# Kernel tuning notes

Measured on AMD Instinct MI355X. Metric: run time of the kernel, lower is better.

The kernel has to match this reference:

```python
import jax, jax.numpy as jnp
import numpy as np

M, N, NNZ, NITER = 1_000_000, 1_000_000, 8_000_000, 5


def setup_inputs() -> dict:
    key = jax.random.key(0)
    ks = jax.random.split(key, 24)
    f32 = jnp.float32
    inp = dict(
        rows=jax.random.randint(ks[0], (NNZ,), 0, M, dtype=jnp.int32),
        cols=jax.random.randint(ks[1], (NNZ,), 0, N, dtype=jnp.int32),
        vals=jax.random.normal(ks[2], (NNZ,), dtype=f32) * 0.1,
        b=jax.random.normal(ks[3], (M, 1), dtype=f32),
        c=jax.random.normal(ks[4], (N, 1), dtype=f32),
        solution=jax.random.normal(ks[5], (N, 1), dtype=f32),
        dual_solution=jax.random.normal(ks[6], (M, 1), dtype=f32),
        x0=jax.random.normal(ks[7], (N, 1), dtype=f32),  # beta=1 init
        y0=jax.random.normal(ks[8], (M, 1), dtype=f32),  # std_y=1 init
        # dual tower: Conv1d(10->4), Conv1d(6->4), update Conv1d(6->1)
        dw1=jax.random.normal(ks[9], (4, 10), dtype=f32) * 0.3,
        db1=jax.random.normal(ks[10], (4,), dtype=f32) * 0.1,
        dw2=jax.random.normal(ks[11], (4, 6), dtype=f32) * 0.3,
        db2=jax.random.normal(ks[12], (4,), dtype=f32) * 0.1,
        dwu=jax.random.normal(ks[13], (1, 6), dtype=f32) * 0.1,
        dbu=jax.random.normal(ks[14], (1,), dtype=f32) * 0.1,
        # primal tower: Conv1d(10->4), Conv1d(6->4), update Conv1d(6->1)
        pw1=jax.random.normal(ks[15], (4, 10), dtype=f32) * 0.3,
        pb1=jax.random.normal(ks[16], (4,), dtype=f32) * 0.1,
        pw2=jax.random.normal(ks[17], (4, 6), dtype=f32) * 0.3,
        pb2=jax.random.normal(ks[18], (4,), dtype=f32) * 0.1,
        pwu=jax.random.normal(ks[19], (1, 6), dtype=f32) * 0.1,
        pbu=jax.random.normal(ks[20], (1,), dtype=f32) * 0.1,
        nb_max_iter=NITER,
    )
    return inp


def reference(rows, cols, vals, b, c, solution, dual_solution, x0, y0,
              dw1, db1, dw2, db2, dwu, dbu,
              pw1, pb1, pw2, pb2, pwu, pbu, nb_max_iter):
    m, n = b.shape[0], c.shape[0]

    def A_mm(X):   # sparse A @ X : [n,k] -> [m,k]
        return jax.ops.segment_sum(vals[:, None] * X[cols], rows, num_segments=m)

    def At_mm(Y):  # sparse A.T @ Y : [m,k] -> [n,k]
        return jax.ops.segment_sum(vals[:, None] * Y[rows], cols, num_segments=n)

    def step(carry, _):
        x, y, x_h, y_h = carry  # x[n,1] y[m,1] x_h[4,n] y_h[4,m]
        # dual update
        r = A_mm(x) - b                                   # [m,1]
        atxh = A_mm(x_h.T)                                # [m,4]
        h = jnp.concatenate([y_h, atxh.T, y.T, r.T], 0)   # [10,m]
        h = jax.nn.relu(dw1 @ h + db1[:, None])           # [4,m]
        h = jnp.concatenate([h, y.T, r.T], 0)             # [6,m]
        y_h = jax.nn.relu(dw2 @ h + db2[:, None])         # [4,m]
        h2 = jnp.concatenate([y_h, y.T, r.T], 0)          # [6,m]
        y = y + (dwu @ h2 + dbu[:, None]).T               # [m,1]
        # primal update
        d = c + At_mm(y)                                  # [n,1]
        atyh = At_mm(y_h.T)                               # [n,4]
        g = jnp.concatenate([x_h, atyh.T, x.T, d.T], 0)   # [10,n]
        g = jax.nn.relu(pw1 @ g + pb1[:, None])           # [4,n]
        g = jnp.concatenate([g, x.T, d.T], 0)             # [6,n]
        x_h = jax.nn.relu(pw2 @ g + pb2[:, None])         # [4,n]
        g2 = jnp.concatenate([x_h, x.T, d.T], 0)          # [6,n]
        x = x + (pwu @ g2 + pbu[:, None]).T               # [n,1]
        dp = jnp.sqrt(jnp.sum((x - solution) ** 2))
        dd = jnp.sqrt(jnp.sum((y - dual_solution) ** 2))
        return (x, y, x_h, y_h), (dp, dd)

    init = (x0, y0,
            jnp.zeros((4, n), dtype=x0.dtype),
            jnp.zeros((4, m), dtype=y0.dtype))
    (x, y, _, _), (dps, dds) = jax.lax.scan(step, init, None, length=nb_max_iter)

    loss_primal = jnp.mean(dps) + 1.0 * jnp.mean(jax.nn.relu(dps[1:] - dps[:-1]))
    loss_dual = jnp.mean(dds) + 1.0 * jnp.mean(jax.nn.relu(dds[1:] - dds[:-1]))
    loss = loss_primal + loss_dual
    return x, y, loss, dps, dds
```

## Files before the change

kernel.cpp:

```cpp
#include <hip/hip_runtime.h>
#include <math.h>


#define NITER 5
#define NBK_SHIFT 9
#define NBK (1 << NBK_SHIFT)
#define NBK_MAX 2048
#define CH 32768
#define SORT_CAP 6144

__device__ __forceinline__ float blockReduceSum(float v) {
#pragma unroll
  for (int off = 32; off > 0; off >>= 1) v += __shfl_down(v, off, 64);
  __shared__ float smem[8];
  const int lane = threadIdx.x & 63;
  const int wid = threadIdx.x >> 6;
  if (lane == 0) smem[wid] = v;
  __syncthreads();
  float r = 0.f;
  if (threadIdx.x == 0) {
    const int nw = (blockDim.x + 63) >> 6;
    for (int w = 0; w < nw; ++w) r += smem[w];
  }
  return r;
}

__global__ __launch_bounds__(1024) void zero_meta(int* __restrict__ cntA,
                                                  int* __restrict__ cntT,
                                                  float* __restrict__ red) {
  const int i = threadIdx.x;
  cntA[i] = 0;
  cntA[i + 1024] = 0;
  cntT[i] = 0;
  cntT[i + 1024] = 0;
  if (i < 16) red[i] = 0.f;
}

__global__ __launch_bounds__(256) void hist2(const int* __restrict__ rows,
                                             const int* __restrict__ cols,
                                             int* __restrict__ cntA,
                                             int* __restrict__ cntT, int nnz) {
  __shared__ int hA[NBK_MAX];
  __shared__ int hT[NBK_MAX];
  for (int i = threadIdx.x; i < NBK_MAX; i += 256) { hA[i] = 0; hT[i] = 0; }
  __syncthreads();
  const int stride = gridDim.x * blockDim.x;
  for (int e = blockIdx.x * blockDim.x + threadIdx.x; e < nnz; e += stride) {
    atomicAdd(&hA[rows[e] >> NBK_SHIFT], 1);
    atomicAdd(&hT[cols[e] >> NBK_SHIFT], 1);
  }
  __syncthreads();
  for (int i = threadIdx.x; i < NBK_MAX; i += 256) {
    if (hA[i]) atomicAdd(&cntA[i], hA[i]);
    if (hT[i]) atomicAdd(&cntT[i], hT[i]);
  }
}

__global__ __launch_bounds__(1024) void scan_bases(const int* __restrict__ cnt,
                                                   int* __restrict__ base,
                                                   int* __restrict__ fill,
                                                   int nb) {
  __shared__ int sm[1024];
  int run = 0;
  for (int s = 0; s < nb; s += 1024) {
    const int i = s + threadIdx.x;
    const int x = (i < nb) ? cnt[i] : 0;
    sm[threadIdx.x] = x;
    __syncthreads();
#pragma unroll
    for (int off = 1; off < 1024; off <<= 1) {
      const int add = (threadIdx.x >= off) ? sm[threadIdx.x - off] : 0;
      __syncthreads();
      sm[threadIdx.x] += add;
      __syncthreads();
    }
    if (i < nb) {
      const int ex = run + sm[threadIdx.x] - x;
      base[i] = ex;
      fill[i] = ex;
    }
    const int tot = sm[1023];
    __syncthreads();
    run += tot;
  }
}

__global__ __launch_bounds__(512) void scatter2(
    const int* __restrict__ rows, const int* __restrict__ cols,
    const float* __restrict__ vals, int* __restrict__ fillA,
    int* __restrict__ fillT, int2* __restrict__ eA, int2* __restrict__ eT,
    int nnz) {
  __shared__ int hA[NBK_MAX];
  __shared__ int hT[NBK_MAX];
  for (int i = threadIdx.x; i < NBK_MAX; i += 512) { hA[i] = 0; hT[i] = 0; }
  __syncthreads();
  const int e0 = blockIdx.x * CH;
  for (int k = threadIdx.x; k < CH; k += 512) {
    const int e = e0 + k;
    if (e < nnz) {
      atomicAdd(&hA[rows[e] >> NBK_SHIFT], 1);
      atomicAdd(&hT[cols[e] >> NBK_SHIFT], 1);
    }
  }
  __syncthreads();
  for (int i = threadIdx.x; i < NBK_MAX; i += 512) {
    const int cA = hA[i];
    if (cA) hA[i] = atomicAdd(&fillA[i], cA);
    const int cT = hT[i];
    if (cT) hT[i] = atomicAdd(&fillT[i], cT);
  }
  __syncthreads();
  for (int k = threadIdx.x; k < CH; k += 512) {
    const int e = e0 + k;
    if (e < nnz) {
      const int r = rows[e];
      const int c = cols[e];
      const int vb = __float_as_int(vals[e]);
      const int pA = atomicAdd(&hA[r >> NBK_SHIFT], 1);
      eA[pA] = make_int2(((r & (NBK - 1)) << 20) | c, vb);
      const int pT = atomicAdd(&hT[c >> NBK_SHIFT], 1);
      eT[pT] = make_int2(((c & (NBK - 1)) << 20) | r, vb);
    }
  }
}

__global__ __launch_bounds__(256) void sort_bucket(const int* __restrict__ base,
                                                   const int* __restrict__ cnt,
                                                   int2* __restrict__ edges) {
  __shared__ int2 recs[SORT_CAP];
  __shared__ int hist[NBK];
  __shared__ int wsum[256];
  const int bkt = blockIdx.x;
  const int beg = base[bkt];
  const int num = cnt[bkt];
  if (num > SORT_CAP) return;
  for (int i = threadIdx.x; i < NBK; i += 256) hist[i] = 0;
  __syncthreads();
  for (int k = threadIdx.x; k < num; k += 256) {
    const int2 r = edges[beg + k];
    recs[k] = r;
    atomicAdd(&hist[((unsigned)r.x) >> 20], 1);
  }
  __syncthreads();
  const int b2 = threadIdx.x * 2;
  const int h0 = hist[b2];
  const int h1 = hist[b2 + 1];
  wsum[threadIdx.x] = h0 + h1;
  __syncthreads();
#pragma unroll
  for (int off = 1; off < 256; off <<= 1) {
    const int add = (threadIdx.x >= off) ? wsum[threadIdx.x - off] : 0;
    __syncthreads();
    wsum[threadIdx.x] += add;
    __syncthreads();
  }
  const int excl = (threadIdx.x == 0) ? 0 : wsum[threadIdx.x - 1];
  __syncthreads();
  hist[b2] = excl;
  hist[b2 + 1] = excl + h0;
  __syncthreads();
  for (int k = threadIdx.x; k < num; k += 256) {
    const int2 r = recs[k];
    const int p = atomicAdd(&hist[((unsigned)r.x) >> 20], 1);
    edges[beg + p] = r;
  }
}

__global__ __launch_bounds__(256) void init_state2(const float* __restrict__ x0,
                                                   const float* __restrict__ y0,
                                                   float* __restrict__ X5,
                                                   float* __restrict__ Y5,
                                                   int n, int m) {
  const int i = blockIdx.x * blockDim.x + threadIdx.x;
  if (i < n) {
    float* xp = X5 + (size_t)i * 8;
    xp[0] = x0[i];
    xp[1] = 0.f; xp[2] = 0.f; xp[3] = 0.f; xp[4] = 0.f;
  }
  if (i < m) {
    float* yp = Y5 + (size_t)i * 8;
    yp[0] = y0[i];
    yp[1] = 0.f; yp[2] = 0.f; yp[3] = 0.f; yp[4] = 0.f;
  }
}

__global__ __launch_bounds__(256) void fused_bucket_tower(
    const int* __restrict__ base, const int* __restrict__ cnt,
    const int2* __restrict__ edges, const float* __restrict__ src,
    float* __restrict__ state, const float* __restrict__ seed, float sign,
    const float* __restrict__ sol, const float* __restrict__ w1,
    const float* __restrict__ b1, const float* __restrict__ w2,
    const float* __restrict__ b2, const float* __restrict__ wu,
    const float* __restrict__ bu, float* __restrict__ red_slot, int count) {
  __shared__ float acc[NBK * 5];
  for (int i = threadIdx.x; i < NBK * 5; i += 256) acc[i] = 0.f;
  __syncthreads();
  const int bkt = blockIdx.x;
  const int beg = base[bkt];
  const int num = cnt[bkt];
  const int lane = threadIdx.x & 63;
  for (int k0 = 0; k0 < num; k0 += 256) {
    const int k = k0 + threadIdx.x;
    int dl = -1;
    float m0 = 0.f, m1 = 0.f, m2 = 0.f, m3 = 0.f, m4 = 0.f;
    if (k < num) {
      const int2 ed = edges[beg + k];
      dl = ((unsigned)ed.x) >> 20;
      const int sc = ed.x & 0xFFFFF;
      const float v = __int_as_float(ed.y);
      const float* sp = src + (size_t)sc * 8;
      const float4 lo = *reinterpret_cast<const float4*>(sp);
      m0 = v * lo.x; m1 = v * lo.y; m2 = v * lo.z; m3 = v * lo.w;
      m4 = v * sp[4];
    }
#pragma unroll
    for (int off = 1; off < 64; off <<= 1) {
      const int dlu = __shfl_up(dl, off, 64);
      const float t0 = __shfl_up(m0, off, 64);
      const float t1 = __shfl_up(m1, off, 64);
      const float t2 = __shfl_up(m2, off, 64);
      const float t3 = __shfl_up(m3, off, 64);
      const float t4 = __shfl_up(m4, off, 64);
      if (lane >= off && dlu == dl) {
        m0 += t0; m1 += t1; m2 += t2; m3 += t3; m4 += t4;
      }
    }
    const int dld = __shfl_down(dl, 1, 64);
    const bool last = (lane == 63) || (dld != dl);
    if (dl >= 0 && last) {
      float* ap = acc + dl * 5;
      atomicAdd(ap + 0, m0);
      atomicAdd(ap + 1, m1);
      atomicAdd(ap + 2, m2);
      atomicAdd(ap + 3, m3);
      atomicAdd(ap + 4, m4);
    }
  }
  __syncthreads();
  float part = 0.f;
  for (int t = threadIdx.x; t < NBK; t += 256) {
    const int row = (bkt << NBK_SHIFT) + t;
    if (row < count) {
      const float* a = acc + t * 5;
      const float r = a[0] + sign * seed[row];
      float* sp = state + (size_t)row * 8;
      const float4 st = *reinterpret_cast<const float4*>(sp);
      const float y = st.x;
      float v[10];
      v[0] = st.y; v[1] = st.z; v[2] = st.w; v[3] = sp[4];
      v[4] = a[1]; v[5] = a[2]; v[6] = a[3]; v[7] = a[4];
      v[8] = y;
      v[9] = r;
      float h[4];
#pragma unroll
      for (int o = 0; o < 4; ++o) {
        float accv = b1[o];
#pragma unroll
        for (int kk = 0; kk < 10; ++kk) accv += w1[o * 10 + kk] * v[kk];
        h[o] = fmaxf(accv, 0.f);
      }
      float hn[4];
#pragma unroll
      for (int o = 0; o < 4; ++o) {
        float accv = b2[o] + w2[o * 6 + 4] * y + w2[o * 6 + 5] * r;
#pragma unroll
        for (int kk = 0; kk < 4; ++kk) accv += w2[o * 6 + kk] * h[kk];
        hn[o] = fmaxf(accv, 0.f);
      }
      const float upd = bu[0] + wu[0] * hn[0] + wu[1] * hn[1] + wu[2] * hn[2] +
                        wu[3] * hn[3] + wu[4] * y + wu[5] * r;
      const float yn = y + upd;
      float4 stn;
      stn.x = yn; stn.y = hn[0]; stn.z = hn[1]; stn.w = hn[2];
      *reinterpret_cast<float4*>(sp) = stn;
      sp[4] = hn[3];
      const float diff = yn - sol[row];
      part += diff * diff;
    }
  }
  const float bs = blockReduceSum(part);
  if (threadIdx.x == 0) unsafeAtomicAdd(red_slot, bs);
}

__global__ __launch_bounds__(256) void finalize2(const float* __restrict__ X5,
                                                 const float* __restrict__ Y5,
                                                 const float* __restrict__ red,
                                                 float* __restrict__ out, int n,
                                                 int m) {
  const int i = blockIdx.x * blockDim.x + threadIdx.x;
  if (i < n) out[i] = X5[(size_t)i * 8];
  if (i < m) out[n + i] = Y5[(size_t)i * 8];
  if (i == 0) {
    float dps[NITER], dds[NITER];
#pragma unroll
    for (int t = 0; t < NITER; ++t) {
      dps[t] = sqrtf(red[t]);
      dds[t] = sqrtf(red[NITER + t]);
    }
    float mp = 0.f, md = 0.f, rp = 0.f, rd = 0.f;
#pragma unroll
    for (int t = 0; t < NITER; ++t) { mp += dps[t]; md += dds[t]; }
#pragma unroll
    for (int t = 1; t < NITER; ++t) {
      rp += fmaxf(dps[t] - dps[t - 1], 0.f);
      rd += fmaxf(dds[t] - dds[t - 1], 0.f);
    }
    out[n + m] = mp / NITER + rp / (NITER - 1) + md / NITER + rd / (NITER - 1);
#pragma unroll
    for (int t = 0; t < NITER; ++t) {
      out[n + m + 1 + t] = dps[t];
      out[n + m + 1 + NITER + t] = dds[t];
    }
  }
}

template <int S>
__global__ __launch_bounds__(256) void init_state(
    const float* __restrict__ x0, const float* __restrict__ y0,
    const float* __restrict__ b, float* __restrict__ X5,
    float* __restrict__ Y5, float* __restrict__ Yacc, float* __restrict__ red,
    int n, int m) {
  const int i = blockIdx.x * blockDim.x + threadIdx.x;
  if (i < 16) red[i] = 0.f;
  if (i < n) {
    float* xp = X5 + (size_t)i * S;
    xp[0] = x0[i];
    xp[1] = 0.f; xp[2] = 0.f; xp[3] = 0.f; xp[4] = 0.f;
  }
  if (i < m) {
    float* yp = Y5 + (size_t)i * S;
    yp[0] = y0[i];
    yp[1] = 0.f; yp[2] = 0.f; yp[3] = 0.f; yp[4] = 0.f;
    float* ya = Yacc + (size_t)i * S;
    ya[0] = -b[i];
    ya[1] = 0.f; ya[2] = 0.f; ya[3] = 0.f; ya[4] = 0.f;
  }
}

template <int S>
__global__ __launch_bounds__(256) void spmm5(const int* __restrict__ gidx,
                                             const int* __restrict__ sidx,
                                             const float* __restrict__ vals,
                                             const float* __restrict__ src,
                                             float* __restrict__ dst, int nnz) {
  const int e = blockIdx.x * blockDim.x + threadIdx.x;
  if (e >= nnz) return;
  const int g = gidx[e];
  const int s = sidx[e];
  const float v = vals[e];
  const float* sp = src + (size_t)g * S;
  float s0, s1, s2, s3, s4;
  if constexpr (S == 8) {
    const float4 lo = *reinterpret_cast<const float4*>(sp);
    s0 = lo.x; s1 = lo.y; s2 = lo.z; s3 = lo.w; s4 = sp[4];
  } else {
    s0 = sp[0]; s1 = sp[1]; s2 = sp[2]; s3 = sp[3]; s4 = sp[4];
  }
  float* dp = dst + (size_t)s * S;
  unsafeAtomicAdd(dp + 0, v * s0);
  unsafeAtomicAdd(dp + 1, v * s1);
  unsafeAtomicAdd(dp + 2, v * s2);
  unsafeAtomicAdd(dp + 3, v * s3);
  unsafeAtomicAdd(dp + 4, v * s4);
}

template <int S>
__global__ __launch_bounds__(256) void tower(
    const float* __restrict__ acc, float* __restrict__ state,
    const float* __restrict__ prep_src, float* __restrict__ prep_dst,
    float sign, const float* __restrict__ sol, const float* __restrict__ w1,
    const float* __restrict__ b1, const float* __restrict__ w2,
    const float* __restrict__ b2, const float* __restrict__ wu,
    const float* __restrict__ bu, float* __restrict__ red_slot, int count,
    int prep_count) {
  const int i = blockIdx.x * blockDim.x + threadIdx.x;
  float part = 0.f;
  if (i < count) {
    const float* a = acc + (size_t)i * S;
    const float r = a[0];
    float* sp = state + (size_t)i * S;
    const float y = sp[0];
    float v[10];
    v[0] = sp[1]; v[1] = sp[2]; v[2] = sp[3]; v[3] = sp[4];
    v[4] = a[1];  v[5] = a[2];  v[6] = a[3];  v[7] = a[4];
    v[8] = y;
    v[9] = r;
    float h[4];
#pragma unroll
    for (int o = 0; o < 4; ++o) {
      float accv = b1[o];
#pragma unroll
      for (int k = 0; k < 10; ++k) accv += w1[o * 10 + k] * v[k];
      h[o] = fmaxf(accv, 0.f);
    }
    float hn[4];
#pragma unroll
    for (int o = 0; o < 4; ++o) {
      float accv = b2[o] + w2[o * 6 + 4] * y + w2[o * 6 + 5] * r;
#pragma unroll
      for (int k = 0; k < 4; ++k) accv += w2[o * 6 + k] * h[k];
      hn[o] = fmaxf(accv, 0.f);
    }
    const float upd = bu[0] + wu[0] * hn[0] + wu[1] * hn[1] + wu[2] * hn[2] +
                      wu[3] * hn[3] + wu[4] * y + wu[5] * r;
    const float yn = y + upd;
    sp[0] = yn;
    sp[1] = hn[0]; sp[2] = hn[1]; sp[3] = hn[2]; sp[4] = hn[3];
    const float diff = yn - sol[i];
    part = diff * diff;
  }
  if (i < prep_count) {
    float* pd = prep_dst + (size_t)i * S;
    pd[0] = sign * prep_src[i];
    pd[1] = 0.f; pd[2] = 0.f; pd[3] = 0.f; pd[4] = 0.f;
  }
  const float bs = blockReduceSum(part);
  if (threadIdx.x == 0) unsafeAtomicAdd(red_slot, bs);
}

template <int S>
static void run_atomic(const int* rows, const int* cols, const float* vals,
                       const float* b, const float* c, const float* solution,
                       const float* dual_solution, const float* x0,
                       const float* y0, const float* dw1, const float* db1,
                       const float* dw2, const float* db2, const float* dwu,
                       const float* dbu, const float* pw1, const float* pb1,
                       const float* pw2, const float* pb2, const float* pwu,
                       const float* pbu, float* out, float* ws, int n, int m,
                       int nnz, hipStream_t stream) {
  float* X5 = ws;
  float* Y5 = X5 + (size_t)n * S;
  float* Xacc = Y5 + (size_t)m * S;
  float* Yacc = Xacc + (size_t)n * S;
  float* red = Yacc + (size_t)m * S;

  const int BLK = 256;
  const int nm = (n > m) ? n : m;
  const int gN = (nm + BLK - 1) / BLK;
  const int gE = (nnz + BLK - 1) / BLK;

  init_state<S><<<gN, BLK, 0, stream>>>(x0, y0, b, X5, Y5, Yacc, red, n, m);
  for (int t = 0; t < NITER; ++t) {
    spmm5<S><<<gE, BLK, 0, stream>>>(cols, rows, vals, X5, Yacc, nnz);
    tower<S><<<gN, BLK, 0, stream>>>(Yacc, Y5, c, Xacc, 1.0f, dual_solution,
                                     dw1, db1, dw2, db2, dwu, dbu,
                                     red + NITER + t, m, n);
    spmm5<S><<<gE, BLK, 0, stream>>>(rows, cols, vals, Y5, Xacc, nnz);
    tower<S><<<gN, BLK, 0, stream>>>(Xacc, X5, b, Yacc, -1.0f, solution, pw1,
                                     pb1, pw2, pb2, pwu, pbu, red + t, n, m);
  }
  finalize2<<<gN, BLK, 0, stream>>>(X5, Y5, red, out, n, m);
}

static inline size_t alignUp(size_t x, size_t a) { return (x + a - 1) / a * a; }

extern "C" void kernel_launch(void* const* d_in, const int* in_sizes, int n_in,
                              void* d_out, int out_size, void* d_ws,
                              size_t ws_size, hipStream_t stream) {
  const int* rows = (const int*)d_in[0];
  const int* cols = (const int*)d_in[1];
  const float* vals = (const float*)d_in[2];
  const float* b = (const float*)d_in[3];
  const float* c = (const float*)d_in[4];
  const float* solution = (const float*)d_in[5];
  const float* dual_solution = (const float*)d_in[6];
  const float* x0 = (const float*)d_in[7];
  const float* y0 = (const float*)d_in[8];
  const float* dw1 = (const float*)d_in[9];
  const float* db1 = (const float*)d_in[10];
  const float* dw2 = (const float*)d_in[11];
  const float* db2 = (const float*)d_in[12];
  const float* dwu = (const float*)d_in[13];
  const float* dbu = (const float*)d_in[14];
  const float* pw1 = (const float*)d_in[15];
  const float* pb1 = (const float*)d_in[16];
  const float* pw2 = (const float*)d_in[17];
  const float* pb2 = (const float*)d_in[18];
  const float* pwu = (const float*)d_in[19];
  const float* pbu = (const float*)d_in[20];

  const int nnz = in_sizes[0];
  const int m = in_sizes[3];
  const int n = in_sizes[4];
  float* out = (float*)d_out;
  char* ws = (char*)d_ws;

  const int nbA = (m + NBK - 1) >> NBK_SHIFT;
  const int nbT = (n + NBK - 1) >> NBK_SHIFT;

  size_t off = 0;
  const size_t oX5 = off;    off = alignUp(off + (size_t)n * 8 * 4, 256);
  const size_t oY5 = off;    off = alignUp(off + (size_t)m * 8 * 4, 256);
  const size_t oEA = off;    off = alignUp(off + (size_t)nnz * 8, 256);
  const size_t oET = off;    off = alignUp(off + (size_t)nnz * 8, 256);
  const size_t oCntA = off;  off = alignUp(off + (size_t)NBK_MAX * 4, 256);
  const size_t oBasA = off;  off = alignUp(off + (size_t)NBK_MAX * 4, 256);
  const size_t oFilA = off;  off = alignUp(off + (size_t)NBK_MAX * 4, 256);
  const size_t oCntT = off;  off = alignUp(off + (size_t)NBK_MAX * 4, 256);
  const size_t oBasT = off;  off = alignUp(off + (size_t)NBK_MAX * 4, 256);
  const size_t oFilT = off;  off = alignUp(off + (size_t)NBK_MAX * 4, 256);
  const size_t oRed = off;   off = alignUp(off + 16 * 4, 256);
  const size_t needB = off;

  const bool ok = (nbA <= NBK_MAX) && (nbT <= NBK_MAX) && (m <= (1 << 20)) &&
                  (n <= (1 << 20)) && (ws_size >= needB);

  if (ok) {
    float* X5 = (float*)(ws + oX5);
    float* Y5 = (float*)(ws + oY5);
    int2* eA = (int2*)(ws + oEA);
    int2* eT = (int2*)(ws + oET);
    int* cntA = (int*)(ws + oCntA);
    int* basA = (int*)(ws + oBasA);
    int* filA = (int*)(ws + oFilA);
    int* cntT = (int*)(ws + oCntT);
    int* basT = (int*)(ws + oBasT);
    int* filT = (int*)(ws + oFilT);
    float* red = (float*)(ws + oRed);

    const int BLK = 256;
    const int nm = (n > m) ? n : m;
    const int gN = (nm + BLK - 1) / BLK;
    const int gC = (nnz + CH - 1) / CH;

    zero_meta<<<1, 1024, 0, stream>>>(cntA, cntT, red);
    hist2<<<256, BLK, 0, stream>>>(rows, cols, cntA, cntT, nnz);
    scan_bases<<<1, 1024, 0, stream>>>(cntA, basA, filA, nbA);
    scan_bases<<<1, 1024, 0, stream>>>(cntT, basT, filT, nbT);
    scatter2<<<gC, 512, 0, stream>>>(rows, cols, vals, filA, filT, eA, eT,
                                     nnz);
    sort_bucket<<<nbA, BLK, 0, stream>>>(basA, cntA, eA);
    sort_bucket<<<nbT, BLK, 0, stream>>>(basT, cntT, eT);
    init_state2<<<gN, BLK, 0, stream>>>(x0, y0, X5, Y5, n, m);

    for (int t = 0; t < NITER; ++t) {
      fused_bucket_tower<<<nbA, BLK, 0, stream>>>(
          basA, cntA, eA, X5, Y5, b, -1.0f, dual_solution, dw1, db1, dw2, db2,
          dwu, dbu, red + NITER + t, m);
      fused_bucket_tower<<<nbT, BLK, 0, stream>>>(
          basT, cntT, eT, Y5, X5, c, 1.0f, solution, pw1, pb1, pw2, pb2, pwu,
          pbu, red + t, n);
    }
    finalize2<<<gN, BLK, 0, stream>>>(X5, Y5, red, out, n, m);
    return;
  }

  const size_t need8 =
      ((size_t)n * 8 + (size_t)m * 8) * 2 * sizeof(float) + 64 * sizeof(float);
  if (ws_size >= need8) {
    run_atomic<8>(rows, cols, vals, b, c, solution, dual_solution, x0, y0, dw1,
                  db1, dw2, db2, dwu, dbu, pw1, pb1, pw2, pb2, pwu, pbu, out,
                  (float*)d_ws, n, m, nnz, stream);
  } else {
    run_atomic<5>(rows, cols, vals, b, c, solution, dual_solution, x0, y0, dw1,
                  db1, dw2, db2, dwu, dbu, pw1, pb1, pw2, pb2, pwu, pbu, out,
                  (float*)d_ws, n, m, nnz, stream);
  }
}
```

Measured before the change: 2.311 ms.

## Replace bucket shared-memory reduction with CSR row-per-thread SpMV tower kernel

The bucket sort now also writes a full CSR row pointer array. This lets the per-iteration tower kernel assign one row to each thread and accumulate its neighbors in registers, replacing the per-bucket wave segmented scan and shared-memory atomics. The sort kernel moves to 512 threads with a single-pass scan over 512 bins, and the chunk size, sort capacity and histogram grid are retuned. The risk is that buckets exceeding the sort capacity never write their row pointers, and row-per-thread traversal can suffer load imbalance on skewed rows.

```diff
diff --git a/kernel.cpp b/kernel.cpp
--- a/kernel.cpp
+++ b/kernel.cpp
@@ -6,8 +6,8 @@
 #define NBK_SHIFT 9
 #define NBK (1 << NBK_SHIFT)
 #define NBK_MAX 2048
-#define CH 32768
-#define SORT_CAP 6144
+#define CH 16384
+#define SORT_CAP 7168
 
 __device__ __forceinline__ float blockReduceSum(float v) {
 #pragma unroll
@@ -124,42 +124,43 @@
   }
 }
 
-__global__ __launch_bounds__(256) void sort_bucket(const int* __restrict__ base,
+__global__ __launch_bounds__(512) void sort_bucket(const int* __restrict__ base,
                                                    const int* __restrict__ cnt,
-                                                   int2* __restrict__ edges) {
+                                                   int2* __restrict__ edges,
+                                                   int* __restrict__ rowptr,
+                                                   int nnz_total) {
   __shared__ int2 recs[SORT_CAP];
   __shared__ int hist[NBK];
-  __shared__ int wsum[256];
   const int bkt = blockIdx.x;
   const int beg = base[bkt];
   const int num = cnt[bkt];
+  if (bkt == 0 && threadIdx.x == 0)
+    rowptr[(int)gridDim.x << NBK_SHIFT] = nnz_total;
   if (num > SORT_CAP) return;
-  for (int i = threadIdx.x; i < NBK; i += 256) hist[i] = 0;
-  __syncthreads();
-  for (int k = threadIdx.x; k < num; k += 256) {
+  hist[threadIdx.x] = 0;
+  __syncthreads();
+  for (int k = threadIdx.x; k < num; k += 512) {
     const int2 r = edges[beg + k];
     recs[k] = r;
     atomicAdd(&hist[((unsigned)r.x) >> 20], 1);
   }
   __syncthreads();
-  const int b2 = threadIdx.x * 2;
-  const int h0 = hist[b2];
-  const int h1 = hist[b2 + 1];
-  wsum[threadIdx.x] = h0 + h1;
-  __syncthreads();
-#pragma unroll
-  for (int off = 1; off < 256; off <<= 1) {
-    const int add = (threadIdx.x >= off) ? wsum[threadIdx.x - off] : 0;
+  const int x = hist[threadIdx.x];
+  int incl = x;
+#pragma unroll
+  for (int off = 1; off < NBK; off <<= 1) {
+    int add = 0;
+    if (threadIdx.x >= off) add = hist[threadIdx.x - off];
     __syncthreads();
-    wsum[threadIdx.x] += add;
+    incl += add;
+    hist[threadIdx.x] = incl;
     __syncthreads();
   }
-  const int excl = (threadIdx.x == 0) ? 0 : wsum[threadIdx.x - 1];
-  __syncthreads();
-  hist[b2] = excl;
-  hist[b2 + 1] = excl + h0;
-  __syncthreads();
-  for (int k = threadIdx.x; k < num; k += 256) {
+  const int excl = incl - x;
+  hist[threadIdx.x] = excl;
+  rowptr[(bkt << NBK_SHIFT) + threadIdx.x] = beg + excl;
+  __syncthreads();
+  for (int k = threadIdx.x; k < num; k += 512) {
     const int2 r = recs[k];
     const int p = atomicAdd(&hist[((unsigned)r.x) >> 20], 1);
     edges[beg + p] = r;
@@ -184,99 +185,79 @@
   }
 }
 
-__global__ __launch_bounds__(256) void fused_bucket_tower(
-    const int* __restrict__ base, const int* __restrict__ cnt,
-    const int2* __restrict__ edges, const float* __restrict__ src,
-    float* __restrict__ state, const float* __restrict__ seed, float sign,
-    const float* __restrict__ sol, const float* __restrict__ w1,
-    const float* __restrict__ b1, const float* __restrict__ w2,
-    const float* __restrict__ b2, const float* __restrict__ wu,
-    const float* __restrict__ bu, float* __restrict__ red_slot, int count) {
-  __shared__ float acc[NBK * 5];
-  for (int i = threadIdx.x; i < NBK * 5; i += 256) acc[i] = 0.f;
-  __syncthreads();
-  const int bkt = blockIdx.x;
-  const int beg = base[bkt];
-  const int num = cnt[bkt];
-  const int lane = threadIdx.x & 63;
-  for (int k0 = 0; k0 < num; k0 += 256) {
-    const int k = k0 + threadIdx.x;
-    int dl = -1;
-    float m0 = 0.f, m1 = 0.f, m2 = 0.f, m3 = 0.f, m4 = 0.f;
-    if (k < num) {
-      const int2 ed = edges[beg + k];
-      dl = ((unsigned)ed.x) >> 20;
-      const int sc = ed.x & 0xFFFFF;
-      const float v = __int_as_float(ed.y);
-      const float* sp = src + (size_t)sc * 8;
-      const float4 lo = *reinterpret_cast<const float4*>(sp);
-      m0 = v * lo.x; m1 = v * lo.y; m2 = v * lo.z; m3 = v * lo.w;
-      m4 = v * sp[4];
-    }
-#pragma unroll
-    for (int off = 1; off < 64; off <<= 1) {
-      const int dlu = __shfl_up(dl, off, 64);
-      const float t0 = __shfl_up(m0, off, 64);
-      const float t1 = __shfl_up(m1, off, 64);
-      const float t2 = __shfl_up(m2, off, 64);
-      const float t3 = __shfl_up(m3, off, 64);
-      const float t4 = __shfl_up(m4, off, 64);
-      if (lane >= off && dlu == dl) {
-        m0 += t0; m1 += t1; m2 += t2; m3 += t3; m4 += t4;
-      }
-    }
-    const int dld = __shfl_down(dl, 1, 64);
-    const bool last = (lane == 63) || (dld != dl);
-    if (dl >= 0 && last) {
-      float* ap = acc + dl * 5;
-      atomicAdd(ap + 0, m0);
-      atomicAdd(ap + 1, m1);
-      atomicAdd(ap + 2, m2);
-      atomicAdd(ap + 3, m3);
-      atomicAdd(ap + 4, m4);
-    }
-  }
-  __syncthreads();
+__global__ __launch_bounds__(256) void csr_tower(
+    const int* __restrict__ rowptr, const int2* __restrict__ edges,
+    const float* __restrict__ src, float* __restrict__ state,
+    const float* __restrict__ seed, float sign, const float* __restrict__ sol,
+    const float* __restrict__ w1, const float* __restrict__ b1,
+    const float* __restrict__ w2, const float* __restrict__ b2,
+    const float* __restrict__ wu, const float* __restrict__ bu,
+    float* __restrict__ red_slot, int count) {
+  const int i = blockIdx.x * blockDim.x + threadIdx.x;
   float part = 0.f;
-  for (int t = threadIdx.x; t < NBK; t += 256) {
-    const int row = (bkt << NBK_SHIFT) + t;
-    if (row < count) {
-      const float* a = acc + t * 5;
-      const float r = a[0] + sign * seed[row];
-      float* sp = state + (size_t)row * 8;
-      const float4 st = *reinterpret_cast<const float4*>(sp);
-      const float y = st.x;
-      float v[10];
-      v[0] = st.y; v[1] = st.z; v[2] = st.w; v[3] = sp[4];
-      v[4] = a[1]; v[5] = a[2]; v[6] = a[3]; v[7] = a[4];
-      v[8] = y;
-      v[9] = r;
-      float h[4];
-#pragma unroll
-      for (int o = 0; o < 4; ++o) {
-        float accv = b1[o];
-#pragma unroll
-        for (int kk = 0; kk < 10; ++kk) accv += w1[o * 10 + kk] * v[kk];
-        h[o] = fmaxf(accv, 0.f);
-      }
-      float hn[4];
-#pragma unroll
-      for (int o = 0; o < 4; ++o) {
-        float accv = b2[o] + w2[o * 6 + 4] * y + w2[o * 6 + 5] * r;
-#pragma unroll
-        for (int kk = 0; kk < 4; ++kk) accv += w2[o * 6 + kk] * h[kk];
-        hn[o] = fmaxf(accv, 0.f);
-      }
-      const float upd = bu[0] + wu[0] * hn[0] + wu[1] * hn[1] + wu[2] * hn[2] +
-                        wu[3] * hn[3] + wu[4] * y + wu[5] * r;
-      const float yn = y + upd;
-      float4 stn;
-      stn.x = yn; stn.y = hn[0]; stn.z = hn[1]; stn.w = hn[2];
-      *reinterpret_cast<float4*>(sp) = stn;
-      sp[4] = hn[3];
-      const float diff = yn - sol[row];
-      part += diff * diff;
-    }
+  if (i < count) {
+    const int rp0 = rowptr[i];
+    const int rp1 = rowptr[i + 1];
+    float a0 = 0.f, a1 = 0.f, a2 = 0.f, a3 = 0.f, a4 = 0.f;
+    int k = rp0;
+    for (; k + 2 <= rp1; k += 2) {
+      const int2 e0 = edges[k];
+      const int2 e1 = edges[k + 1];
+      const float* s0 = src + (size_t)(e0.x & 0xFFFFF) * 8;
+      const float* s1 = src + (size_t)(e1.x & 0xFFFFF) * 8;
+      const float4 l0 = *reinterpret_cast<const float4*>(s0);
+      const float4 l1 = *reinterpret_cast<const float4*>(s1);
+      const float f40 = s0[4];
+      const float f41 = s1[4];
+      const float v0 = __int_as_float(e0.y);
+      const float v1 = __int_as_float(e1.y);
+      a0 += v0 * l0.x; a1 += v0 * l0.y; a2 += v0 * l0.z; a3 += v0 * l0.w;
+      a4 += v0 * f40;
+      a0 += v1 * l1.x; a1 += v1 * l1.y; a2 += v1 * l1.z; a3 += v1 * l1.w;
+      a4 += v1 * f41;
+    }
+    if (k < rp1) {
+      const int2 e0 = edges[k];
+      const float* s0 = src + (size_t)(e0.x & 0xFFFFF) * 8;
+      const float4 l0 = *reinterpret_cast<const float4*>(s0);
+      const float v0 = __int_as_float(e0.y);
+      a0 += v0 * l0.x; a1 += v0 * l0.y; a2 += v0 * l0.z; a3 += v0 * l0.w;
+      a4 += v0 * s0[4];
+    }
+    const float r = a0 + sign * seed[i];
+    float* sp = state + (size_t)i * 8;
+    const float4 st = *reinterpret_cast<const float4*>(sp);
+    const float y = st.x;
+    float v[10];
+    v[0] = st.y; v[1] = st.z; v[2] = st.w; v[3] = sp[4];
+    v[4] = a1; v[5] = a2; v[6] = a3; v[7] = a4;
+    v[8] = y;
+    v[9] = r;
+    float h[4];
+#pragma unroll
+    for (int o = 0; o < 4; ++o) {
+      float accv = b1[o];
+#pragma unroll
+      for (int kk = 0; kk < 10; ++kk) accv += w1[o * 10 + kk] * v[kk];
+      h[o] = fmaxf(accv, 0.f);
+    }
+    float hn[4];
+#pragma unroll
+    for (int o = 0; o < 4; ++o) {
+      float accv = b2[o] + w2[o * 6 + 4] * y + w2[o * 6 + 5] * r;
+#pragma unroll
+      for (int kk = 0; kk < 4; ++kk) accv += w2[o * 6 + kk] * h[kk];
+      hn[o] = fmaxf(accv, 0.f);
+    }
+    const float upd = bu[0] + wu[0] * hn[0] + wu[1] * hn[1] + wu[2] * hn[2] +
+                      wu[3] * hn[3] + wu[4] * y + wu[5] * r;
+    const float yn = y + upd;
+    float4 stn;
+    stn.x = yn; stn.y = hn[0]; stn.z = hn[1]; stn.w = hn[2];
+    *reinterpret_cast<float4*>(sp) = stn;
+    sp[4] = hn[3];
+    const float diff = yn - sol[i];
+    part = diff * diff;
   }
   const float bs = blockReduceSum(part);
   if (threadIdx.x == 0) unsafeAtomicAdd(red_slot, bs);
@@ -493,6 +474,8 @@
   const size_t oY5 = off;    off = alignUp(off + (size_t)m * 8 * 4, 256);
   const size_t oEA = off;    off = alignUp(off + (size_t)nnz * 8, 256);
   const size_t oET = off;    off = alignUp(off + (size_t)nnz * 8, 256);
+  const size_t oRpA = off;   off = alignUp(off + ((size_t)nbA * NBK + 1) * 4, 256);
+  const size_t oRpT = off;   off = alignUp(off + ((size_t)nbT * NBK + 1) * 4, 256);
   const size_t oCntA = off;  off = alignUp(off + (size_t)NBK_MAX * 4, 256);
   const size_t oBasA = off;  off = alignUp(off + (size_t)NBK_MAX * 4, 256);
   const size_t oFilA = off;  off = alignUp(off + (size_t)NBK_MAX * 4, 256);
@@ -510,6 +493,8 @@
     float* Y5 = (float*)(ws + oY5);
     int2* eA = (int2*)(ws + oEA);
     int2* eT = (int2*)(ws + oET);
+    int* rpA = (int*)(ws + oRpA);
+    int* rpT = (int*)(ws + oRpT);
     int* cntA = (int*)(ws + oCntA);
     int* basA = (int*)(ws + oBasA);
     int* filA = (int*)(ws + oFilA);
@@ -521,25 +506,27 @@
     const int BLK = 256;
     const int nm = (n > m) ? n : m;
     const int gN = (nm + BLK - 1) / BLK;
+    const int gM = (m + BLK - 1) / BLK;
+    const int gNn = (n + BLK - 1) / BLK;
     const int gC = (nnz + CH - 1) / CH;
 
     zero_meta<<<1, 1024, 0, stream>>>(cntA, cntT, red);
-    hist2<<<256, BLK, 0, stream>>>(rows, cols, cntA, cntT, nnz);
+    hist2<<<512, BLK, 0, stream>>>(rows, cols, cntA, cntT, nnz);
     scan_bases<<<1, 1024, 0, stream>>>(cntA, basA, filA, nbA);
     scan_bases<<<1, 1024, 0, stream>>>(cntT, basT, filT, nbT);
     scatter2<<<gC, 512, 0, stream>>>(rows, cols, vals, filA, filT, eA, eT,
                                      nnz);
-    sort_bucket<<<nbA, BLK, 0, stream>>>(basA, cntA, eA);
-    sort_bucket<<<nbT, BLK, 0, stream>>>(basT, cntT, eT);
+    sort_bucket<<<nbA, 512, 0, stream>>>(basA, cntA, eA, rpA, nnz);
+    sort_bucket<<<nbT, 512, 0, stream>>>(basT, cntT, eT, rpT, nnz);
     init_state2<<<gN, BLK, 0, stream>>>(x0, y0, X5, Y5, n, m);
 
     for (int t = 0; t < NITER; ++t) {
-      fused_bucket_tower<<<nbA, BLK, 0, stream>>>(
-          basA, cntA, eA, X5, Y5, b, -1.0f, dual_solution, dw1, db1, dw2, db2,
-          dwu, dbu, red + NITER + t, m);
-      fused_bucket_tower<<<nbT, BLK, 0, stream>>>(
-          basT, cntT, eT, Y5, X5, c, 1.0f, solution, pw1, pb1, pw2, pb2, pwu,
-          pbu, red + t, n);
+      csr_tower<<<gM, BLK, 0, stream>>>(rpA, eA, X5, Y5, b, -1.0f,
+                                        dual_solution, dw1, db1, dw2, db2, dwu,
+                                        dbu, red + NITER + t, m);
+      csr_tower<<<gNn, BLK, 0, stream>>>(rpT, eT, Y5, X5, c, 1.0f, solution,
+                                         pw1, pb1, pw2, pb2, pwu, pbu, red + t,
+                                         n);
     }
     finalize2<<<gN, BLK, 0, stream>>>(X5, Y5, red, out, n, m);
     return;
```

New measurement: 2.517 ms. +8.9%, slower.
